# Kernel optimization log

Hardware: AMD Instinct MI355X
Metric: run time of the kernel (lower is better)

Reference implementation:

```python
import jax, jax.numpy as jnp
import numpy as np

DIM = 3072
NUM_HEADS = 24
HEAD_DIM = DIM // NUM_HEADS  # 128
SEQ = 2048
BATCH = 1


def rms_norm(x, scale):
    # compute in fp32 like the torch module
    xf = x.astype(jnp.float32)
    rrms = jax.lax.rsqrt(jnp.mean(xf * xf, axis=-1, keepdims=True) + 1e-6)
    return (xf * rrms).astype(x.dtype) * scale


def apply_rope(xq, xk, pe):
    # xq, xk: [B, H, L, D]; pe: [B, 1, L, D//2, 2, 2]
    shp = xq.shape
    xq_ = xq.reshape(*shp[:-1], -1, 1, 2).astype(jnp.float32)
    xk_ = xk.reshape(*shp[:-1], -1, 1, 2).astype(jnp.float32)
    xq_out = pe[..., 0] * xq_[..., 0] + pe[..., 1] * xq_[..., 1]
    xk_out = pe[..., 0] * xk_[..., 0] + pe[..., 1] * xk_[..., 1]
    return xq_out.reshape(shp).astype(xq.dtype), xk_out.reshape(shp).astype(xk.dtype)


def setup_inputs() -> dict:
    key = jax.random.key(0)
    ks = jax.random.split(key, 6)
    s = 1.0 / np.sqrt(DIM)
    return {
        "x": jax.random.normal(ks[0], (BATCH, SEQ, DIM), dtype=jnp.float32),
        "pe": jax.random.normal(ks[1], (BATCH, 1, SEQ, HEAD_DIM // 2, 2, 2), dtype=jnp.float32),
        "w_qkv": jax.random.normal(ks[2], (3 * DIM, DIM), dtype=jnp.float32) * s,
        "w_proj": jax.random.normal(ks[3], (DIM, DIM), dtype=jnp.float32) * s,
        "b_proj": jax.random.normal(ks[4], (DIM,), dtype=jnp.float32) * 0.01,
        "q_scale": jnp.ones((HEAD_DIM,), dtype=jnp.float32),
        "k_scale": jnp.ones((HEAD_DIM,), dtype=jnp.float32),
    }


def reference(x, pe, w_qkv, w_proj, b_proj, q_scale, k_scale):
    B, L, _ = x.shape
    # fused qkv projection (qkv_bias=False)
    qkv = jnp.einsum("bld,ed->ble", x, w_qkv)  # [B, L, 3*DIM]
    qkv = qkv.reshape(B, L, 3, NUM_HEADS, HEAD_DIM)
    qkv = jnp.transpose(qkv, (2, 0, 3, 1, 4))  # [3, B, H, L, D]
    q, k, v = qkv[0], qkv[1], qkv[2]
    # QKNorm (RMSNorm on head_dim)
    q = rms_norm(q, q_scale).astype(v.dtype)
    k = rms_norm(k, k_scale).astype(v.dtype)
    # rope
    q, k = apply_rope(q, k, pe)
    # scaled dot-product attention
    scale = 1.0 / np.sqrt(HEAD_DIM)
    scores = jnp.einsum("bhqd,bhkd->bhqk", q, k) * scale
    probs = jax.nn.softmax(scores, axis=-1)
    out = jnp.einsum("bhqk,bhkd->bhqd", probs, v)
    out = jnp.transpose(out, (0, 2, 1, 3)).reshape(B, L, DIM)  # merge heads
    # output projection
    return jnp.einsum("bld,ed->ble", out, w_proj) + b_proj
```

## Files before the change

kernel.cpp:

```cpp
#include <hip/hip_runtime.h>

typedef __bf16 bf16;
typedef __attribute__((ext_vector_type(8))) __bf16 bf16x8;
typedef __attribute__((ext_vector_type(4))) float f32x4;

typedef __attribute__((address_space(1))) void gvoid_t;
typedef __attribute__((address_space(3))) void lvoid_t;

#define LDS_LOAD16(gp, lp) \
    __builtin_amdgcn_global_load_lds((gvoid_t*)(gp), (lvoid_t*)(lp), 16, 0, 0)

__global__ __launch_bounds__(256)
void f32_to_bf16(const float* __restrict__ in, bf16* __restrict__ out, int n8)
{
    const int i = blockIdx.x * 256 + threadIdx.x;
    if (i >= n8) return;
    const float4 a = ((const float4*)in)[i * 2];
    const float4 b = ((const float4*)in)[i * 2 + 1];
    bf16x8 o;
    o[0] = (bf16)a.x; o[1] = (bf16)a.y; o[2] = (bf16)a.z; o[3] = (bf16)a.w;
    o[4] = (bf16)b.x; o[5] = (bf16)b.y; o[6] = (bf16)b.z; o[7] = (bf16)b.w;
    *(bf16x8*)(out + (size_t)i * 8) = o;
}

template <int BIAS, typename CT>
__global__ __launch_bounds__(256, 2)
void gemm_bt(const bf16* __restrict__ A, const bf16* __restrict__ B,
             const float* __restrict__ bias, CT* __restrict__ C,
             int K, int ldc)
{
    __shared__ bf16 sA[128 * 32];
    __shared__ bf16 sB[128 * 32];
    const int tid  = threadIdx.x;
    const int lane = tid & 63;
    const int wid  = tid >> 6;
    const int m0 = blockIdx.y * 128;
    const int n0 = blockIdx.x * 128;
    const int wm = (wid >> 1) * 64;
    const int wn = (wid & 1) * 64;
    const int l15   = lane & 15;
    const int quad8 = (lane >> 4) * 8;

    f32x4 acc[4][4] = {};

    for (int k0 = 0; k0 < K; k0 += 32) {
#pragma unroll
        for (int t = 0; t < 2; ++t) {
            const int e  = (t * 4 + wid) * 512;
            const int ge = e + lane * 8;
            const int r = ge >> 5, c = ge & 31;
            LDS_LOAD16(A + (size_t)(m0 + r) * K + k0 + c, sA + e);
            LDS_LOAD16(B + (size_t)(n0 + r) * K + k0 + c, sB + e);
        }
        __syncthreads();

        bf16x8 af[4], bfr[4];
#pragma unroll
        for (int i = 0; i < 4; ++i) {
            af[i]  = *(const bf16x8*)(sA + (wm + i * 16 + l15) * 32 + quad8);
            bfr[i] = *(const bf16x8*)(sB + (wn + i * 16 + l15) * 32 + quad8);
        }
#pragma unroll
        for (int i = 0; i < 4; ++i)
#pragma unroll
            for (int j = 0; j < 4; ++j)
                acc[i][j] = __builtin_amdgcn_mfma_f32_16x16x32_bf16(af[i], bfr[j], acc[i][j], 0, 0, 0);
        __syncthreads();
    }

    const int rowBase = m0 + wm + (lane >> 4) * 4;
    const int colBase = n0 + wn + l15;
#pragma unroll
    for (int j = 0; j < 4; ++j) {
        const int col = colBase + j * 16;
        const float bv = BIAS ? bias[col] : 0.0f;
#pragma unroll
        for (int i = 0; i < 4; ++i) {
            const int row = rowBase + i * 16;
#pragma unroll
            for (int r = 0; r < 4; ++r)
                C[(size_t)(row + r) * ldc + col] = (CT)(acc[i][j][r] + bv);
        }
    }
}

template <int BIAS, typename CT>
__global__ __launch_bounds__(512, 2)
void gemm256_bt(const bf16* __restrict__ A, const bf16* __restrict__ B,
                const float* __restrict__ bias, CT* __restrict__ C,
                int K, int ldc)
{
    __shared__ bf16 sA[2 * 256 * 64];
    __shared__ bf16 sB[2 * 192 * 64];

    const int tid  = threadIdx.x;
    const int lane = tid & 63;
    const int wid  = tid >> 6;
    const int m0 = blockIdx.y * 256;
    const int n0 = blockIdx.x * 192;
    const int wm = (wid >> 2) * 128;
    const int wn = (wid & 3) * 48;
    const int l15  = lane & 15;
    const int quad = lane >> 4;
    const int swz  = l15 & 7;

    int aoff[4], boff[3];
    int adst[4], bdst[3];
#pragma unroll
    for (int t = 0; t < 4; ++t) {
        const int slot = t * 512 + tid;
        const int r  = slot >> 3;
        const int cg = (slot & 7) ^ (r & 7);
        aoff[t] = (m0 + r) * K + cg * 8;
        adst[t] = (t * 512 + wid * 64) * 8;
    }
#pragma unroll
    for (int t = 0; t < 3; ++t) {
        const int slot = t * 512 + tid;
        const int r  = slot >> 3;
        const int cg = (slot & 7) ^ (r & 7);
        boff[t] = (n0 + r) * K + cg * 8;
        bdst[t] = (t * 512 + wid * 64) * 8;
    }

#define STA(t, kt, buf) LDS_LOAD16(A + (size_t)aoff[t] + (kt) * 64, sA + (buf) * 16384 + adst[t])
#define STB(t, kt, buf) LDS_LOAD16(B + (size_t)boff[t] + (kt) * 64, sB + (buf) * 12288 + bdst[t])

    int aRd[2], bRd[2];
#pragma unroll
    for (int kk = 0; kk < 2; ++kk) {
        const int pcg = (kk * 4 + quad) ^ swz;
        aRd[kk] = (wm + l15) * 128 + pcg * 16;
        bRd[kk] = (wn + l15) * 128 + pcg * 16;
    }

    f32x4 acc[8][3] = {};
    bf16x8 bfrag[3][2];

#pragma unroll
    for (int t = 0; t < 3; ++t) STB(t, 0, 0);
#pragma unroll
    for (int t = 0; t < 4; ++t) STA(t, 0, 0);
#pragma unroll
    for (int t = 0; t < 3; ++t) STB(t, 1, 1);
    asm volatile("s_waitcnt vmcnt(3)" ::: "memory");
    __builtin_amdgcn_s_barrier();

#define GRP_PHASE(p, gb, STAGE_STMT, WAITC)                                         \
    {                                                                               \
        bf16x8 af[2][2];                                                            \
        _Pragma("unroll")                                                           \
        for (int mi = 0; mi < 2; ++mi)                                              \
            _Pragma("unroll")                                                       \
            for (int kk = 0; kk < 2; ++kk)                                          \
                af[mi][kk] = *(const bf16x8*)((const char*)sA + (gb) * 32768 +      \
                                              aRd[kk] + ((p) * 2 + mi) * 2048);     \
        if ((p) == 0) {                                                             \
            _Pragma("unroll")                                                       \
            for (int nf = 0; nf < 3; ++nf)                                          \
                _Pragma("unroll")                                                   \
                for (int kk = 0; kk < 2; ++kk)                                      \
                    bfrag[nf][kk] = *(const bf16x8*)((const char*)sB + (gb) * 24576 \
                                                     + bRd[kk] + nf * 2048);        \
        }                                                                           \
        STAGE_STMT;                                                                 \
        __builtin_amdgcn_s_barrier();                                               \
        asm volatile("s_waitcnt lgkmcnt(0)" ::: "memory");                          \
        __builtin_amdgcn_sched_barrier(0);                                          \
        __builtin_amdgcn_s_setprio(1);                                              \
        _Pragma("unroll")                                                           \
        for (int mi = 0; mi < 2; ++mi)                                              \
            _Pragma("unroll")                                                       \
            for (int nf = 0; nf < 3; ++nf)                                          \
                _Pragma("unroll")                                                   \
                for (int kk = 0; kk < 2; ++kk)                                      \
                    acc[(p) * 2 + mi][nf] = __builtin_amdgcn_mfma_f32_16x16x32_bf16(\
                        af[mi][kk], bfrag[nf][kk], acc[(p) * 2 + mi][nf], 0, 0, 0); \
        __builtin_amdgcn_s_setprio(0);                                              \
        __builtin_amdgcn_sched_barrier(0);                                          \
        WAITC;                                                                      \
        __builtin_amdgcn_s_barrier();                                               \
    }

    const int NT = K >> 6;
#pragma unroll 1
    for (int u = 0; u < NT; u += 2) {
        const int t_o  = u + 1;
        const int t_e2 = (u + 2 < NT) ? u + 2 : NT - 1;
        const int t_o2 = (u + 3 < NT) ? u + 3 : NT - 1;
        GRP_PHASE(0, 0, { STA(0, t_o, 1); STA(1, t_o, 1); }, )
        GRP_PHASE(1, 0, { STA(2, t_o, 1); STA(3, t_o, 1); }, )
        GRP_PHASE(2, 0, { STB(0, t_e2, 0); }, )
        GRP_PHASE(3, 0, { STB(1, t_e2, 0); STB(2, t_e2, 0); },
                  asm volatile("s_waitcnt vmcnt(3)" ::: "memory"))
        GRP_PHASE(0, 1, { STA(0, t_e2, 0); STA(1, t_e2, 0); }, )
        GRP_PHASE(1, 1, { STA(2, t_e2, 0); STA(3, t_e2, 0); }, )
        GRP_PHASE(2, 1, { STB(0, t_o2, 1); }, )
        GRP_PHASE(3, 1, { STB(1, t_o2, 1); STB(2, t_o2, 1); },
                  asm volatile("s_waitcnt vmcnt(3)" ::: "memory"))
    }
#undef GRP_PHASE
#undef STA
#undef STB

    asm volatile("s_waitcnt vmcnt(0)" ::: "memory");

    const int rowBase = m0 + wm + quad * 4;
    const int colBase = n0 + wn + l15;
#pragma unroll
    for (int nf = 0; nf < 3; ++nf) {
        const int col = colBase + nf * 16;
        const float bv = BIAS ? bias[col] : 0.0f;
#pragma unroll
        for (int mf = 0; mf < 8; ++mf) {
            const int row = rowBase + mf * 16;
#pragma unroll
            for (int r = 0; r < 4; ++r)
                C[(size_t)(row + r) * ldc + col] = (CT)(acc[mf][nf][r] + bv);
        }
    }
}

__global__ __launch_bounds__(256)
void qk_rope_rearrange(const bf16* __restrict__ qkv, const float* __restrict__ pe,
                       const float* __restrict__ qs, const float* __restrict__ ks,
                       bf16* __restrict__ Qh, bf16* __restrict__ Kh, bf16* __restrict__ Vt)
{
    const int lane = threadIdx.x & 63;
    const int wid  = threadIdx.x >> 6;
    const int idx  = blockIdx.x * 4 + wid;
    const int h = idx >> 11;
    const int l = idx & 2047;

    const size_t rowb = (size_t)l * 9216 + h * 128 + 2 * lane;
    const float q0 = (float)qkv[rowb];
    const float q1 = (float)qkv[rowb + 1];
    const float k0 = (float)qkv[rowb + 3072];
    const float k1 = (float)qkv[rowb + 3073];
    const bf16  v0 = qkv[rowb + 6144];
    const bf16  v1 = qkv[rowb + 6145];

    float ssq = q0 * q0 + q1 * q1;
    float ssk = k0 * k0 + k1 * k1;
#pragma unroll
    for (int off = 1; off < 64; off <<= 1) {
        ssq += __shfl_xor(ssq, off);
        ssk += __shfl_xor(ssk, off);
    }
    const float rq = rsqrtf(ssq * (1.0f / 128.0f) + 1e-6f);
    const float rk = rsqrtf(ssk * (1.0f / 128.0f) + 1e-6f);

    const float s0q = qs[2 * lane], s1q = qs[2 * lane + 1];
    const float s0k = ks[2 * lane], s1k = ks[2 * lane + 1];

    const float qn0 = (q0 * rq) * s0q;
    const float qn1 = (q1 * rq) * s1q;
    const float kn0 = (k0 * rk) * s0k;
    const float kn1 = (k1 * rk) * s1k;

    const float* pp = pe + ((size_t)l * 64 + lane) * 4;
    const float p00 = pp[0], p01 = pp[1];
    const float p10 = pp[2], p11 = pp[3];

    const bf16 qo0 = (bf16)(p00 * qn0 + p01 * qn1);
    const bf16 qo1 = (bf16)(p10 * qn0 + p11 * qn1);
    const bf16 ko0 = (bf16)(p00 * kn0 + p01 * kn1);
    const bf16 ko1 = (bf16)(p10 * kn0 + p11 * kn1);

    const size_t ob = ((size_t)h * 2048 + l) * 128 + 2 * lane;
    Qh[ob] = qo0; Qh[ob + 1] = qo1;
    Kh[ob] = ko0; Kh[ob + 1] = ko1;

    const size_t vb = ((size_t)h * 128 + 2 * lane) * 2048 + l;
    Vt[vb]        = v0;
    Vt[vb + 2048] = v1;
}

__global__ __launch_bounds__(256, 2)
void flash_attn(const bf16* __restrict__ Qh, const bf16* __restrict__ Kh,
                const bf16* __restrict__ Vt, bf16* __restrict__ AO)
{
    __shared__ bf16 sK[2 * 64 * 128];
    __shared__ bf16 sV[2 * 128 * 64];
    __shared__ bf16 sP[4 * 16 * 72];

    const int tid   = threadIdx.x;
    const int lane  = tid & 63;
    const int wid   = tid >> 6;
    const int h     = blockIdx.y;
    const int qw    = blockIdx.x * 64 + wid * 16;
    const int l15   = lane & 15;
    const int quad  = lane >> 4;
    const int quad8 = quad * 8;

    const bf16* Kbase = Kh + (size_t)h * 2048 * 128;
    const bf16* Vbase = Vt + (size_t)h * 128 * 2048;

    bf16x8 aq[4];
    {
        const bf16* qp = Qh + ((size_t)h * 2048 + qw + l15) * 128 + quad8;
#pragma unroll
        for (int ki = 0; ki < 4; ++ki) aq[ki] = *(const bf16x8*)(qp + ki * 32);
    }

    bf16x8 ones;
#pragma unroll
    for (int i = 0; i < 8; ++i) ones[i] = (bf16)1.0f;

    f32x4 o[8] = {};
    f32x4 lacc = {};

    bf16* sPw = sP + wid * (16 * 72);
    const int slotbase = wid * 64;

#define STAGE_K(kv, buf)                                                         \
    {                                                                            \
        bf16* kb = sK + (buf) * (64 * 128);                                      \
        _Pragma("unroll")                                                        \
        for (int t = 0; t < 4; ++t) {                                            \
            const int sb   = t * 256 + slotbase;                                 \
            const int slot = sb + lane;                                          \
            const int r    = slot >> 4;                                          \
            const int cg   = (slot & 15) ^ (r & 7);                              \
            LDS_LOAD16(Kbase + (size_t)((kv) + r) * 128 + cg * 8, kb + sb * 8);  \
        }                                                                        \
    }
#define STAGE_V(kv, buf)                                                         \
    {                                                                            \
        bf16* vb = sV + (buf) * (128 * 64);                                      \
        _Pragma("unroll")                                                        \
        for (int t = 0; t < 4; ++t) {                                            \
            const int sb   = t * 256 + slotbase;                                 \
            const int slot = sb + lane;                                          \
            const int r    = slot >> 3;                                          \
            const int cg   = (slot & 7) ^ (r & 7);                               \
            LDS_LOAD16(Vbase + (size_t)r * 2048 + (kv) + cg * 8, vb + sb * 8);   \
        }                                                                        \
    }

    STAGE_K(0, 0);
    STAGE_V(0, 0);

    for (int s = 0; s < 32; ++s) {
        __syncthreads();
        if (s < 31) {
            STAGE_K((s + 1) * 64, (s + 1) & 1);
            STAGE_V((s + 1) * 64, (s + 1) & 1);
        }

        const bf16* kb = sK + (s & 1) * (64 * 128);
        const bf16* vb = sV + (s & 1) * (128 * 64);

        f32x4 sc[4];
#pragma unroll
        for (int nt = 0; nt < 4; ++nt) {
            f32x4 t = {};
            const int row = nt * 16 + l15;
#pragma unroll
            for (int ki = 0; ki < 4; ++ki) {
                const int pcg = (4 * ki + quad) ^ (l15 & 7);
                bf16x8 bk = *(const bf16x8*)(kb + row * 128 + pcg * 8);
                t = __builtin_amdgcn_mfma_f32_16x16x32_bf16(aq[ki], bk, t, 0, 0, 0);
            }
            sc[nt] = t;
        }

#pragma unroll
        for (int r = 0; r < 4; ++r) {
            const float scl = 0.08838834764831845f;
            bf16* pw = sPw + (quad * 4 + r) * 72 + l15;
            pw[0]  = (bf16)__expf(sc[0][r] * scl);
            pw[16] = (bf16)__expf(sc[1][r] * scl);
            pw[32] = (bf16)__expf(sc[2][r] * scl);
            pw[48] = (bf16)__expf(sc[3][r] * scl);
        }

#pragma unroll
        for (int kk = 0; kk < 2; ++kk) {
            bf16x8 pa = *(const bf16x8*)(sPw + l15 * 72 + kk * 32 + quad8);
            lacc = __builtin_amdgcn_mfma_f32_16x16x32_bf16(pa, ones, lacc, 0, 0, 0);
#pragma unroll
            for (int dt = 0; dt < 8; ++dt) {
                const int row = dt * 16 + l15;
                const int pcg = (kk * 4 + quad) ^ (l15 & 7);
                bf16x8 bv = *(const bf16x8*)(vb + row * 64 + pcg * 8);
                o[dt] = __builtin_amdgcn_mfma_f32_16x16x32_bf16(pa, bv, o[dt], 0, 0, 0);
            }
        }
    }
#undef STAGE_K
#undef STAGE_V

#pragma unroll
    for (int r = 0; r < 4; ++r) {
        const float inv = 1.0f / lacc[r];
        const size_t row = qw + quad * 4 + r;
        bf16* op = AO + row * 3072 + h * 128 + l15;
#pragma unroll
        for (int dt = 0; dt < 8; ++dt) op[dt * 16] = (bf16)(o[dt][r] * inv);
    }
}

extern "C" void kernel_launch(void* const* d_in, const int* in_sizes, int n_in,
                              void* d_out, int out_size, void* d_ws, size_t ws_size,
                              hipStream_t stream)
{
    (void)in_sizes; (void)n_in; (void)out_size;

    const float* x      = (const float*)d_in[0];
    const float* pe     = (const float*)d_in[1];
    const float* w_qkv  = (const float*)d_in[2];
    const float* w_proj = (const float*)d_in[3];
    const float* b_proj = (const float*)d_in[4];
    const float* q_s    = (const float*)d_in[5];
    const float* k_s    = (const float*)d_in[6];
    float* out = (float*)d_out;

    const size_t NEED_BIG = ((size_t)6291456 + 28311552 + 18874368 + 6291456) * 2;

    if (ws_size >= NEED_BIG) {
        bf16* xb  = (bf16*)d_ws;
        bf16* wb  = xb + (size_t)6291456;
        bf16* qkv = wb + (size_t)28311552;
        bf16* Vt  = qkv + (size_t)18874368;
        bf16* Qh  = xb;
        bf16* Kh  = wb;
        bf16* wpb = qkv;
        bf16* AO  = qkv + (size_t)9437184;

        f32_to_bf16<<<dim3(3072),  256, 0, stream>>>(x,     xb, 786432);
        f32_to_bf16<<<dim3(13824), 256, 0, stream>>>(w_qkv, wb, 3538944);
        gemm256_bt<0, bf16><<<dim3(48, 8), 512, 0, stream>>>(xb, wb, nullptr, qkv, 3072, 9216);
        qk_rope_rearrange<<<dim3(12288), 256, 0, stream>>>(qkv, pe, q_s, k_s, Qh, Kh, Vt);
        f32_to_bf16<<<dim3(4608), 256, 0, stream>>>(w_proj, wpb, 1179648);
        flash_attn<<<dim3(32, 24), 256, 0, stream>>>(Qh, Kh, Vt, AO);
        gemm_bt<1, float><<<dim3(24, 16), 256, 0, stream>>>(AO, wpb, b_proj, out, 3072, 3072);
    } else {
        bf16* xb  = (bf16*)d_ws;
        bf16* wb  = xb + (size_t)6291456;
        bf16* qkv = wb + (size_t)9437184;
        bf16* Vt  = qkv + (size_t)18874368;
        bf16* Qh  = xb;
        bf16* Kh  = wb;
        bf16* wpb = qkv;
        bf16* AO  = qkv + (size_t)9437184;

        f32_to_bf16<<<dim3(3072), 256, 0, stream>>>(x, xb, 786432);
        for (int c = 0; c < 3; ++c) {
            f32_to_bf16<<<dim3(4608), 256, 0, stream>>>(w_qkv + (size_t)c * 9437184, wb, 1179648);
            gemm_bt<0, bf16><<<dim3(24, 16), 256, 0, stream>>>(xb, wb, nullptr, qkv + c * 3072, 3072, 9216);
        }
        qk_rope_rearrange<<<dim3(12288), 256, 0, stream>>>(qkv, pe, q_s, k_s, Qh, Kh, Vt);
        f32_to_bf16<<<dim3(4608), 256, 0, stream>>>(w_proj, wpb, 1179648);
        flash_attn<<<dim3(32, 24), 256, 0, stream>>>(Qh, Kh, Vt, AO);
        gemm_bt<1, float><<<dim3(24, 16), 256, 0, stream>>>(AO, wpb, b_proj, out, 3072, 3072);
    }
}
```

Measured before the change: 572.3 us.

## Triple-buffer A tile in GEMM to deepen global-to-LDS prefetch

The A operand gets a third LDS buffer, so A tiles are prefetched two k-steps ahead instead of one. The main loop is rotated over three A buffers, unrolling six k-tiles per iteration, and the vmcnt waits are relaxed from 3 to 7 so more loads stay in flight. The goal is to hide global load latency behind MFMA work. The cost is 32 KB more LDS per block, which may cut occupancy below the two blocks per CU requested in launch bounds. The loop also assumes NT is a multiple of six.

```diff
diff --git a/kernel.cpp b/kernel.cpp
--- a/kernel.cpp
+++ b/kernel.cpp
@@ -90,7 +90,7 @@
                 const float* __restrict__ bias, CT* __restrict__ C,
                 int K, int ldc)
 {
-    __shared__ bf16 sA[2 * 256 * 64];
+    __shared__ bf16 sA[3 * 256 * 64];
     __shared__ bf16 sB[2 * 192 * 64];
 
     const int tid  = threadIdx.x;
@@ -138,29 +138,31 @@
     bf16x8 bfrag[3][2];
 
 #pragma unroll
+    for (int t = 0; t < 4; ++t) STA(t, 0, 0);
+#pragma unroll
     for (int t = 0; t < 3; ++t) STB(t, 0, 0);
 #pragma unroll
-    for (int t = 0; t < 4; ++t) STA(t, 0, 0);
+    for (int t = 0; t < 4; ++t) STA(t, 1, 1);
 #pragma unroll
     for (int t = 0; t < 3; ++t) STB(t, 1, 1);
-    asm volatile("s_waitcnt vmcnt(3)" ::: "memory");
+    asm volatile("s_waitcnt vmcnt(7)" ::: "memory");
     __builtin_amdgcn_s_barrier();
 
-#define GRP_PHASE(p, gb, STAGE_STMT, WAITC)                                         \
+#define GRP_PHASE(p, ab, bb, STAGE_STMT, WAITC)                                     \
     {                                                                               \
         bf16x8 af[2][2];                                                            \
         _Pragma("unroll")                                                           \
         for (int mi = 0; mi < 2; ++mi)                                              \
             _Pragma("unroll")                                                       \
             for (int kk = 0; kk < 2; ++kk)                                          \
-                af[mi][kk] = *(const bf16x8*)((const char*)sA + (gb) * 32768 +      \
+                af[mi][kk] = *(const bf16x8*)((const char*)sA + (ab) * 32768 +      \
                                               aRd[kk] + ((p) * 2 + mi) * 2048);     \
         if ((p) == 0) {                                                             \
             _Pragma("unroll")                                                       \
             for (int nf = 0; nf < 3; ++nf)                                          \
                 _Pragma("unroll")                                                   \
                 for (int kk = 0; kk < 2; ++kk)                                      \
-                    bfrag[nf][kk] = *(const bf16x8*)((const char*)sB + (gb) * 24576 \
+                    bfrag[nf][kk] = *(const bf16x8*)((const char*)sB + (bb) * 24576 \
                                                      + bRd[kk] + nf * 2048);        \
         }                                                                           \
         STAGE_STMT;                                                                 \
@@ -175,30 +177,38 @@
                 _Pragma("unroll")                                                   \
                 for (int kk = 0; kk < 2; ++kk)                                      \
                     acc[(p) * 2 + mi][nf] = __builtin_amdgcn_mfma_f32_16x16x32_bf16(\
-                        af[mi][kk], bfrag[nf][kk], acc[(p) * 2 + mi][nf], 0, 0, 0); \
+                        af[mi][kk], bfrag[nf][kk], acc[(p) * 2 + mi][kk == 0 ? nf : nf], 0, 0, 0); \
         __builtin_amdgcn_s_setprio(0);                                              \
         __builtin_amdgcn_sched_barrier(0);                                          \
         WAITC;                                                                      \
         __builtin_amdgcn_s_barrier();                                               \
     }
 
+#define VM7 asm volatile("s_waitcnt vmcnt(7)" ::: "memory")
+
+#define ITER(u, A0i, A1i, A2i)                                               \
+    {                                                                        \
+        const int ke = ((u) + 2 < NT) ? (u) + 2 : NT - 1;                    \
+        const int ko = ((u) + 3 < NT) ? (u) + 3 : NT - 1;                    \
+        GRP_PHASE(0, A0i, 0, { STA(0, ke, A2i); STA(1, ke, A2i); }, )        \
+        GRP_PHASE(1, A0i, 0, { STA(2, ke, A2i); STA(3, ke, A2i); }, )        \
+        GRP_PHASE(2, A0i, 0, { STB(0, ke, 0); }, )                           \
+        GRP_PHASE(3, A0i, 0, { STB(1, ke, 0); STB(2, ke, 0); }, VM7)         \
+        GRP_PHASE(0, A1i, 1, { STA(0, ko, A0i); STA(1, ko, A0i); }, )        \
+        GRP_PHASE(1, A1i, 1, { STA(2, ko, A0i); STA(3, ko, A0i); }, )        \
+        GRP_PHASE(2, A1i, 1, { STB(0, ko, 1); }, )                           \
+        GRP_PHASE(3, A1i, 1, { STB(1, ko, 1); STB(2, ko, 1); }, VM7)         \
+    }
+
     const int NT = K >> 6;
 #pragma unroll 1
-    for (int u = 0; u < NT; u += 2) {
-        const int t_o  = u + 1;
-        const int t_e2 = (u + 2 < NT) ? u + 2 : NT - 1;
-        const int t_o2 = (u + 3 < NT) ? u + 3 : NT - 1;
-        GRP_PHASE(0, 0, { STA(0, t_o, 1); STA(1, t_o, 1); }, )
-        GRP_PHASE(1, 0, { STA(2, t_o, 1); STA(3, t_o, 1); }, )
-        GRP_PHASE(2, 0, { STB(0, t_e2, 0); }, )
-        GRP_PHASE(3, 0, { STB(1, t_e2, 0); STB(2, t_e2, 0); },
-                  asm volatile("s_waitcnt vmcnt(3)" ::: "memory"))
-        GRP_PHASE(0, 1, { STA(0, t_e2, 0); STA(1, t_e2, 0); }, )
-        GRP_PHASE(1, 1, { STA(2, t_e2, 0); STA(3, t_e2, 0); }, )
-        GRP_PHASE(2, 1, { STB(0, t_o2, 1); }, )
-        GRP_PHASE(3, 1, { STB(1, t_o2, 1); STB(2, t_o2, 1); },
-                  asm volatile("s_waitcnt vmcnt(3)" ::: "memory"))
-    }
+    for (int u6 = 0; u6 < NT; u6 += 6) {
+        ITER(u6 + 0, 0, 1, 2)
+        ITER(u6 + 2, 2, 0, 1)
+        ITER(u6 + 4, 1, 2, 0)
+    }
+#undef ITER
+#undef VM7
 #undef GRP_PHASE
 #undef STA
 #undef STB
```

New measurement: 580.9 us. No clear change (+1.5%).
